# Optimization experiments

Hardware: AMD Instinct MI355X
Metric: run time of the kernel (lower is better)

The kernel has to match this reference:

```python
import jax, jax.numpy as jnp
import numpy as np

B, D_IN, T = 16, 1024, 4096
CB_SIZE, CB_DIM = 8192, 512
EPS = 1e-12


def _conv1d_s2(x, w):
    # x: [b, c_in, t], w: [c_out, c_in, 3]; stride 2, padding 1 (matches nn.Conv1d)
    return jax.lax.conv_general_dilated(
        x, w, window_strides=(2,), padding=[(1, 1)],
        dimension_numbers=("NCH", "OIH", "NCH"))


def _l2_normalize(v):
    # F.normalize(v, dim=1) semantics
    return v / jnp.maximum(jnp.linalg.norm(v, axis=1, keepdims=True), EPS)


def setup_inputs() -> dict:
    key = jax.random.key(0)
    k1, k2, k3, k4 = jax.random.split(key, 4)
    x = jax.random.normal(k1, (B, D_IN, T), dtype=jnp.float32)
    w1 = jax.random.normal(k2, (CB_DIM, D_IN, 3), dtype=jnp.float32) * 0.02
    w2 = jax.random.normal(k3, (CB_DIM, CB_DIM, 3), dtype=jnp.float32) * 0.02
    codebook = jax.random.normal(k4, (CB_SIZE, CB_DIM), dtype=jnp.float32)
    return {"x": x, "w1": w1, "w2": w2, "codebook": codebook}


def reference(x, w1, w2, codebook):
    # in_proj: two stride-2 convs -> [b, cb_dim, t], t = T // 4
    x_e = _conv1d_s2(_conv1d_s2(x, w1), w2)
    b, d, t = x_e.shape
    enc = x_e.transpose(0, 2, 1).reshape(b * t, d)   # (b t) d
    enc = _l2_normalize(enc)
    cb = _l2_normalize(codebook)
    # squared euclidean distance via matmul
    dist = (jnp.sum(enc * enc, axis=1, keepdims=True)
            - 2.0 * enc @ cb.T
            + jnp.sum(cb * cb, axis=1)[None, :])     # (b t) codebook_size
    indices = jnp.argmax(-dist, axis=1).reshape(b, t)
    return indices
```

## Files before the change

### kernel.cpp

```cpp
#include <hip/hip_runtime.h>


typedef __attribute__((ext_vector_type(8))) _Float16 f16x8;
typedef __attribute__((ext_vector_type(8))) short bf16x8;
typedef __attribute__((ext_vector_type(4))) float f32x4;

__device__ inline ushort f2bf(float x) {
  union { float f; unsigned u; } v; v.f = x;
  unsigned r = v.u + 0x7fffu + ((v.u >> 16) & 1u);
  return (ushort)(r >> 16);
}

__device__ inline void splitf(float v, ushort& h, ushort& l) {
  union { _Float16 h; ushort u; } a, b;
  a.h = (_Float16)v;
  b.h = (_Float16)(v - (float)a.h);
  h = a.u; l = b.u;
}

__global__ __launch_bounds__(256) void prep_w(const float* __restrict__ w,
                                              ushort* __restrict__ ws,
                                              int n ) {
  const int idx = blockIdx.x * 256 + threadIdx.x;
  if (idx >= n) return;
  const float v0 = w[(size_t)idx * 3 + 0];
  const float v1 = w[(size_t)idx * 3 + 1];
  const float v2 = w[(size_t)idx * 3 + 2];
  ushort h, l;
  splitf(v0, h, l); ws[idx] = h; ws[(size_t)n + idx] = l;
  splitf(v1, h, l); ws[2 * (size_t)n + idx] = h; ws[3 * (size_t)n + idx] = l;
  splitf(v2, h, l); ws[4 * (size_t)n + idx] = h; ws[5 * (size_t)n + idx] = l;
}

template <int C_IN, int T_IN, int T_OUT, bool TOUT>
__global__ __launch_bounds__(256, 3) void conv_mfma(
    const float* __restrict__ x, const ushort* __restrict__ ws,
    float* __restrict__ out) {
  const int co0 = blockIdx.x * 128;
  const int t0 = blockIdx.y * 128;
  const int b = blockIdx.z;
  const int tid = threadIdx.x;
  const int wv = tid >> 6;
  const int lane = tid & 63;
  const int l15 = lane & 15, quad = lane >> 4;

  constexpr int PX = 40;
  __shared__ ushort xe_hi[128 * PX], xe_lo[128 * PX];
  __shared__ ushort xo_hi[130 * PX], xo_lo[130 * PX];

  f32x4 acc[2][8] = {};
  const float* xb = x + (size_t)b * C_IN * T_IN;

  for (int ci0 = 0; ci0 < C_IN; ci0 += 32) {
    __syncthreads();
    {
      const int cg = tid & 3, tf = tid >> 2;
#pragma unroll
      for (int r = 0; r < 8; r++) {
        const int ci = cg * 8 + r;
        const float* xp = xb + (size_t)(ci0 + ci) * T_IN + 2 * t0 + 4 * tf;
        const float4 v = *(const float4*)xp;
        ushort h, l;
        splitf(v.x, h, l); xe_hi[(2 * tf) * PX + ci] = h; xe_lo[(2 * tf) * PX + ci] = l;
        splitf(v.y, h, l); xo_hi[(2 * tf + 1) * PX + ci] = h; xo_lo[(2 * tf + 1) * PX + ci] = l;
        splitf(v.z, h, l); xe_hi[(2 * tf + 1) * PX + ci] = h; xe_lo[(2 * tf + 1) * PX + ci] = l;
        splitf(v.w, h, l); xo_hi[(2 * tf + 2) * PX + ci] = h; xo_lo[(2 * tf + 2) * PX + ci] = l;
        if (tf == 0) {
          const float v0 = (t0 > 0) ? xp[-1] : 0.0f;
          splitf(v0, h, l); xo_hi[ci] = h; xo_lo[ci] = l;
        }
      }
    }
    __syncthreads();

#pragma unroll
    for (int koff = 0; koff < 3; koff++) {
      f16x8 a_h[2], a_l[2];
#pragma unroll
      for (int i = 0; i < 2; i++) {
        const size_t co = (size_t)co0 + wv * 32 + i * 16 + l15;
        const ushort* wp = ws + ((size_t)(koff * 2) * 512 + co) * C_IN + ci0 + quad * 8;
        a_h[i] = *(const f16x8*)wp;
        a_l[i] = *(const f16x8*)(wp + (size_t)512 * C_IN);
      }
      const ushort* bh_arr = (koff == 1) ? xe_hi : xo_hi;
      const ushort* bl_arr = (koff == 1) ? xe_lo : xo_lo;
      const int radd = (koff == 2) ? 1 : 0;
#pragma unroll
      for (int j = 0; j < 8; j++) {
        const int row = j * 16 + l15 + radd;
        const f16x8 b_h = *(const f16x8*)(bh_arr + row * PX + quad * 8);
        const f16x8 b_l = *(const f16x8*)(bl_arr + row * PX + quad * 8);
#pragma unroll
        for (int i = 0; i < 2; i++) {
          acc[i][j] = __builtin_amdgcn_mfma_f32_16x16x32_f16(a_h[i], b_h, acc[i][j], 0, 0, 0);
          acc[i][j] = __builtin_amdgcn_mfma_f32_16x16x32_f16(a_h[i], b_l, acc[i][j], 0, 0, 0);
          acc[i][j] = __builtin_amdgcn_mfma_f32_16x16x32_f16(a_l[i], b_h, acc[i][j], 0, 0, 0);
        }
      }
    }
  }

#pragma unroll
  for (int i = 0; i < 2; i++) {
#pragma unroll
    for (int j = 0; j < 8; j++) {
      const int t = t0 + j * 16 + l15;
      const int co = co0 + wv * 32 + i * 16 + quad * 4;
      if (TOUT) {
        const float4 v = make_float4(acc[i][j][0], acc[i][j][1], acc[i][j][2], acc[i][j][3]);
        *(float4*)(out + ((size_t)b * T_OUT + t) * 512 + co) = v;
      } else {
#pragma unroll
        for (int r = 0; r < 4; r++)
          out[((size_t)b * 512 + co + r) * T_OUT + t] = acc[i][j][r];
      }
    }
  }
}

__global__ __launch_bounds__(64) void norm_rows(const float* __restrict__ out2t,
                                                float* __restrict__ enc,
                                                ushort* __restrict__ enc16) {
  const int row = blockIdx.x;
  const int lane = threadIdx.x;
  const float* p = out2t + (size_t)row * 512 + lane * 8;
  const float4 v0 = *(const float4*)p;
  const float4 v1 = *(const float4*)(p + 4);
  float ss = v0.x * v0.x + v0.y * v0.y + v0.z * v0.z + v0.w * v0.w +
             v1.x * v1.x + v1.y * v1.y + v1.z * v1.z + v1.w * v1.w;
#pragma unroll
  for (int m = 32; m >= 1; m >>= 1) ss += __shfl_xor(ss, m, 64);
  const float inv = 1.0f / fmaxf(sqrtf(ss), 1e-12f);
  float4 a, c;
  a.x = v0.x * inv; a.y = v0.y * inv; a.z = v0.z * inv; a.w = v0.w * inv;
  c.x = v1.x * inv; c.y = v1.y * inv; c.z = v1.z * inv; c.w = v1.w * inv;
  float* eo = enc + (size_t)row * 512 + lane * 8;
  *(float4*)eo = a;
  *(float4*)(eo + 4) = c;
  ushort u[8] = {f2bf(a.x), f2bf(a.y), f2bf(a.z), f2bf(a.w),
                 f2bf(c.x), f2bf(c.y), f2bf(c.z), f2bf(c.w)};
  *(uint4*)(enc16 + (size_t)row * 512 + lane * 8) = *(const uint4*)u;
}

__global__ __launch_bounds__(256) void norm_cb(const float* __restrict__ cb,
                                               float* __restrict__ cbn,
                                               ushort* __restrict__ cbn16,
                                               float* __restrict__ cb2) {
  const int row = blockIdx.x * 4 + (threadIdx.x >> 6);
  const int lane = threadIdx.x & 63;
  const float* p = cb + (long)row * 512;
  const float4 v0 = *(const float4*)(p + lane * 4);
  const float4 v1 = *(const float4*)(p + 256 + lane * 4);
  float ss = v0.x * v0.x + v0.y * v0.y + v0.z * v0.z + v0.w * v0.w +
             v1.x * v1.x + v1.y * v1.y + v1.z * v1.z + v1.w * v1.w;
#pragma unroll
  for (int m = 32; m >= 1; m >>= 1) ss += __shfl_xor(ss, m, 64);
  const float n = fmaxf(sqrtf(ss), 1e-12f);
  float4 a, c;
  a.x = v0.x / n; a.y = v0.y / n; a.z = v0.z / n; a.w = v0.w / n;
  c.x = v1.x / n; c.y = v1.y / n; c.z = v1.z / n; c.w = v1.w / n;
  *(float4*)(cbn + (long)row * 512 + lane * 4) = a;
  *(float4*)(cbn + (long)row * 512 + 256 + lane * 4) = c;
  ushort4 ua, uc;
  ua.x = f2bf(a.x); ua.y = f2bf(a.y); ua.z = f2bf(a.z); ua.w = f2bf(a.w);
  uc.x = f2bf(c.x); uc.y = f2bf(c.y); uc.z = f2bf(c.z); uc.w = f2bf(c.w);
  *(ushort4*)(cbn16 + (long)row * 512 + lane * 4) = ua;
  *(ushort4*)(cbn16 + (long)row * 512 + 256 + lane * 4) = uc;
  float s2 = a.x * a.x + a.y * a.y + a.z * a.z + a.w * a.w +
             c.x * c.x + c.y * c.y + c.z * c.z + c.w * c.w;
#pragma unroll
  for (int m = 32; m >= 1; m >>= 1) s2 += __shfl_xor(s2, m, 64);
  if (lane == 0) cb2[row] = s2;
}

__device__ inline void top2_merge(float& s1, int& i1, float& s2, int& i2,
                                  float t1, int j1, float t2, int j2) {
  if (t1 > s1) {
    if (s1 > t2) { s2 = s1; i2 = i1; } else { s2 = t2; i2 = j2; }
    s1 = t1; i1 = j1;
  } else if (t1 > s2) {
    s2 = t1; i2 = j1;
  }
}

__global__ __launch_bounds__(256) void score_top2(
    const ushort* __restrict__ enc16, const ushort* __restrict__ cbn16,
    const float* __restrict__ cb2, float* __restrict__ pscore,
    int* __restrict__ pidx) {
  const int nt = blockIdx.x;
  const int mt = blockIdx.y;
  const int m0 = mt * 128, n0 = nt * 128;
  const int tid = threadIdx.x;
  const int wave = tid >> 6, lane = tid & 63;
  const int wm = wave & 1, wn = wave >> 1;
  const int quad = lane >> 4, l15 = lane & 15;

  __shared__ ushort a_s[128 * 72];
  __shared__ ushort b_s[128 * 72];

  f32x4 acc[4][4] = {};

  for (int k0 = 0; k0 < 512; k0 += 64) {
#pragma unroll
    for (int q = 0; q < 4; q++) {
      const int chunk = tid + 256 * q;
      const int row = chunk >> 3, kb = chunk & 7;
      const uint4 va = *(const uint4*)(enc16 + (size_t)(m0 + row) * 512 + k0 + kb * 8);
      *(uint4*)(a_s + row * 72 + kb * 8) = va;
      const uint4 vb = *(const uint4*)(cbn16 + (size_t)(n0 + row) * 512 + k0 + kb * 8);
      *(uint4*)(b_s + row * 72 + kb * 8) = vb;
    }
    __syncthreads();
#pragma unroll
    for (int kk = 0; kk < 2; kk++) {
      bf16x8 af[4], bf[4];
#pragma unroll
      for (int i = 0; i < 4; i++)
        af[i] = *(const bf16x8*)(a_s + (wm * 64 + i * 16 + l15) * 72 + kk * 32 + quad * 8);
#pragma unroll
      for (int j = 0; j < 4; j++)
        bf[j] = *(const bf16x8*)(b_s + (wn * 64 + j * 16 + l15) * 72 + kk * 32 + quad * 8);
#pragma unroll
      for (int i = 0; i < 4; i++)
#pragma unroll
        for (int j = 0; j < 4; j++)
          acc[i][j] = __builtin_amdgcn_mfma_f32_16x16x32_bf16(af[i], bf[j], acc[i][j], 0, 0, 0);
    }
    __syncthreads();
  }

  float cb2c[4];
  int coln[4];
#pragma unroll
  for (int j = 0; j < 4; j++) {
    coln[j] = n0 + wn * 64 + j * 16 + l15;
    cb2c[j] = cb2[coln[j]];
  }

#pragma unroll
  for (int mi = 0; mi < 4; mi++) {
#pragma unroll
    for (int i = 0; i < 4; i++) {
      float s1 = -3.4e38f, s2 = -3.4e38f;
      int i1 = -1, i2 = -1;
#pragma unroll
      for (int j = 0; j < 4; j++) {
        const float s = 2.0f * acc[mi][j][i] - cb2c[j];
        if (s > s1) { s2 = s1; i2 = i1; s1 = s; i1 = coln[j]; }
        else if (s > s2) { s2 = s; i2 = coln[j]; }
      }
#pragma unroll
      for (int m = 8; m >= 1; m >>= 1) {
        const float t1 = __shfl_xor(s1, m, 64);
        const int j1 = __shfl_xor(i1, m, 64);
        const float t2 = __shfl_xor(s2, m, 64);
        const int j2 = __shfl_xor(i2, m, 64);
        top2_merge(s1, i1, s2, i2, t1, j1, t2, j2);
      }
      if (l15 == 0) {
        const int row_g = m0 + wm * 64 + mi * 16 + quad * 4 + i;
        const size_t base = (size_t)row_g * 256 + (size_t)nt * 4 + wn * 2;
        pscore[base] = s1; pidx[base] = i1;
        pscore[base + 1] = s2; pidx[base + 1] = i2;
      }
    }
  }
}

__global__ __launch_bounds__(256) void rescore_argmax(
    const float* __restrict__ enc, const float* __restrict__ cbn,
    const float* __restrict__ cb2, const float* __restrict__ pscore,
    const int* __restrict__ pidx, int* __restrict__ out) {
  const int row = blockIdx.x;
  const int tid = threadIdx.x;
  __shared__ float wbest[4];
  __shared__ int wslot[4];
  __shared__ int winner;
  __shared__ int cand[8];
  __shared__ float fsc[8];
  __shared__ int fid[8];

  float s = pscore[(size_t)row * 256 + tid];
  const int id = pidx[(size_t)row * 256 + tid];

  for (int it = 0; it < 8; it++) {
    float bs = s;
    int bslot = tid;
#pragma unroll
    for (int m = 32; m >= 1; m >>= 1) {
      const float os = __shfl_xor(bs, m, 64);
      const int oslot = __shfl_xor(bslot, m, 64);
      if (os > bs || (os == bs && oslot < bslot)) { bs = os; bslot = oslot; }
    }
    if ((tid & 63) == 0) { wbest[tid >> 6] = bs; wslot[tid >> 6] = bslot; }
    __syncthreads();
    if (tid == 0) {
      float b = wbest[0]; int sl = wslot[0];
      for (int wv = 1; wv < 4; wv++)
        if (wbest[wv] > b || (wbest[wv] == b && wslot[wv] < sl)) { b = wbest[wv]; sl = wslot[wv]; }
      winner = sl;
    }
    __syncthreads();
    if (tid == winner) { cand[it] = id; s = -3.4e38f; }
    __syncthreads();
  }

  const int c = cand[tid >> 5];
  const float* ep = enc + (size_t)row * 512;
  const float* cp = cbn + (size_t)c * 512;
  float dot = 0.0f;
  const int d0 = (tid & 31) * 16;
#pragma unroll
  for (int u = 0; u < 4; u++) {
    const float4 e4 = *(const float4*)(ep + d0 + u * 4);
    const float4 c4 = *(const float4*)(cp + d0 + u * 4);
    dot = fmaf(e4.x, c4.x, dot);
    dot = fmaf(e4.y, c4.y, dot);
    dot = fmaf(e4.z, c4.z, dot);
    dot = fmaf(e4.w, c4.w, dot);
  }
#pragma unroll
  for (int m = 16; m >= 1; m >>= 1) dot += __shfl_xor(dot, m, 64);
  if ((tid & 31) == 0) {
    fsc[tid >> 5] = 2.0f * dot - cb2[c];
    fid[tid >> 5] = c;
  }
  __syncthreads();
  if (tid == 0) {
    float b = fsc[0]; int bi = fid[0];
    for (int q = 1; q < 8; q++)
      if (fsc[q] > b || (fsc[q] == b && fid[q] < bi)) { b = fsc[q]; bi = fid[q]; }
    out[row] = bi;
  }
}

extern "C" void kernel_launch(void* const* d_in, const int* in_sizes, int n_in,
                              void* d_out, int out_size, void* d_ws, size_t ws_size,
                              hipStream_t stream) {
  const float* x = (const float*)d_in[0];
  const float* w1 = (const float*)d_in[1];
  const float* w2 = (const float*)d_in[2];
  const float* cb = (const float*)d_in[3];
  int* out = (int*)d_out;

  char* w0 = (char*)d_ws;
  float* out1 = (float*)w0;
  ushort* enc16 = (ushort*)w0;
  float* pscore = (float*)(w0 + (16ull << 20));
  int* pidx = (int*)(w0 + (32ull << 20));
  float* out2t = (float*)(w0 + (64ull << 20));
  float* enc = (float*)(w0 + (96ull << 20));
  float* cbn = (float*)(w0 + (128ull << 20));
  ushort* cbn16 = (ushort*)(w0 + (144ull << 20));
  float* cb2 = (float*)(w0 + (152ull << 20));
  ushort* ws1 = (ushort*)(w0 + (153ull << 20));
  ushort* ws2 = (ushort*)(w0 + (159ull << 20));

  prep_w<<<2048, 256, 0, stream>>>(w1, ws1, 512 * 1024);
  prep_w<<<1024, 256, 0, stream>>>(w2, ws2, 512 * 512);
  conv_mfma<1024, 4096, 2048, false><<<dim3(4, 16, 16), 256, 0, stream>>>(x, ws1, out1);
  conv_mfma<512, 2048, 1024, true><<<dim3(4, 8, 16), 256, 0, stream>>>(out1, ws2, out2t);
  norm_rows<<<16384, 64, 0, stream>>>(out2t, enc, enc16);
  norm_cb<<<2048, 256, 0, stream>>>(cb, cbn, cbn16, cb2);
  score_top2<<<dim3(64, 128), 256, 0, stream>>>(enc16, cbn16, cb2, pscore, pidx);
  rescore_argmax<<<16384, 256, 0, stream>>>(enc, cbn, cb2, pscore, pidx, out);
}
```

Baseline: 1.917 ms.

## Pre-split conv inputs into fp16 hi/lo even/odd layout and shrink time tile

```diff
diff --git a/kernel.cpp b/kernel.cpp
--- a/kernel.cpp
+++ b/kernel.cpp
@@ -32,43 +32,92 @@
   splitf(v2, h, l); ws[4 * (size_t)n + idx] = h; ws[5 * (size_t)n + idx] = l;
 }
 
-template <int C_IN, int T_IN, int T_OUT, bool TOUT>
-__global__ __launch_bounds__(256, 3) void conv_mfma(
-    const float* __restrict__ x, const ushort* __restrict__ ws,
-    float* __restrict__ out) {
-  const int co0 = blockIdx.x * 128;
-  const int t0 = blockIdx.y * 128;
+__global__ __launch_bounds__(256) void zero_halo(ushort* __restrict__ xo1,
+                                                 ushort* __restrict__ xo2) {
+  const int b = blockIdx.x, tid = threadIdx.x;
+  const uint4 z = make_uint4(0, 0, 0, 0);
+  *(uint4*)(xo1 + (size_t)b * 2049 * 2048 + tid * 8) = z;
+  if (tid < 128) *(uint4*)(xo2 + (size_t)b * 1025 * 1024 + tid * 8) = z;
+}
+
+template <int CI, int T>
+__global__ __launch_bounds__(256) void prep_x(const float* __restrict__ x,
+                                              ushort* __restrict__ xe,
+                                              ushort* __restrict__ xo) {
+  const int t0 = blockIdx.x * 256;
+  const int ci0 = blockIdx.y * 32;
   const int b = blockIdx.z;
   const int tid = threadIdx.x;
-  const int wv = tid >> 6;
-  const int lane = tid & 63;
+  __shared__ float tile[32][257];
+  const int wv = tid >> 6, lane = tid & 63;
+  const float* xb = x + ((size_t)b * CI + ci0) * T + t0;
+#pragma unroll
+  for (int r = 0; r < 8; r++) {
+    const int ci = r * 4 + wv;
+    const float4 v = *(const float4*)(xb + (size_t)ci * T + lane * 4);
+    tile[ci][lane * 4 + 0] = v.x; tile[ci][lane * 4 + 1] = v.y;
+    tile[ci][lane * 4 + 2] = v.z; tile[ci][lane * 4 + 3] = v.w;
+  }
+  __syncthreads();
+  const int jj = tid >> 1, ph = tid & 1;
+  const int tl = 2 * jj + ph;
+  __attribute__((aligned(16))) ushort h[32], l[32];
+#pragma unroll
+  for (int c = 0; c < 32; c++) splitf(tile[c][tl], h[c], l[c]);
+  constexpr int TH = T / 2;
+  constexpr int RW = CI * 2;
+  ushort* dst;
+  if (ph == 0) dst = xe + ((size_t)b * TH + (t0 >> 1) + jj) * RW;
+  else dst = xo + ((size_t)b * (TH + 1) + (t0 >> 1) + jj + 1) * RW;
+  dst += (ci0 >> 5) * 64;
+#pragma unroll
+  for (int k = 0; k < 4; k++) {
+    *(uint4*)(dst + k * 8) = *(const uint4*)(h + k * 8);
+    *(uint4*)(dst + 32 + k * 8) = *(const uint4*)(l + k * 8);
+  }
+}
+
+template <int C_IN, int T_OUT, bool SPLIT_OUT>
+__global__ __launch_bounds__(256, 4) void conv_mfma(
+    const ushort* __restrict__ xe, const ushort* __restrict__ xo,
+    const ushort* __restrict__ ws, float* __restrict__ out,
+    ushort* __restrict__ ye, ushort* __restrict__ yo) {
+  const int co0 = blockIdx.x * 128;
+  const int t0 = blockIdx.y * 64;
+  const int b = blockIdx.z;
+  const int tid = threadIdx.x;
+  const int wv = tid >> 6, lane = tid & 63;
   const int l15 = lane & 15, quad = lane >> 4;
 
-  constexpr int PX = 40;
-  __shared__ ushort xe_hi[128 * PX], xe_lo[128 * PX];
-  __shared__ ushort xo_hi[130 * PX], xo_lo[130 * PX];
-
-  f32x4 acc[2][8] = {};
-  const float* xb = x + (size_t)b * C_IN * T_IN;
+  __shared__ ushort xeh[64 * 40], xel[64 * 40], xoh[65 * 40], xol[65 * 40];
+
+  f32x4 acc[2][4] = {};
+  const int RW = C_IN * 2;
+  const ushort* xe_b = xe + ((size_t)b * T_OUT + t0) * RW;
+  const ushort* xo_b = xo + ((size_t)b * (T_OUT + 1) + t0) * RW;
 
   for (int ci0 = 0; ci0 < C_IN; ci0 += 32) {
     __syncthreads();
-    {
-      const int cg = tid & 3, tf = tid >> 2;
-#pragma unroll
-      for (int r = 0; r < 8; r++) {
-        const int ci = cg * 8 + r;
-        const float* xp = xb + (size_t)(ci0 + ci) * T_IN + 2 * t0 + 4 * tf;
-        const float4 v = *(const float4*)xp;
-        ushort h, l;
-        splitf(v.x, h, l); xe_hi[(2 * tf) * PX + ci] = h; xe_lo[(2 * tf) * PX + ci] = l;
-        splitf(v.y, h, l); xo_hi[(2 * tf + 1) * PX + ci] = h; xo_lo[(2 * tf + 1) * PX + ci] = l;
-        splitf(v.z, h, l); xe_hi[(2 * tf + 1) * PX + ci] = h; xe_lo[(2 * tf + 1) * PX + ci] = l;
-        splitf(v.w, h, l); xo_hi[(2 * tf + 2) * PX + ci] = h; xo_lo[(2 * tf + 2) * PX + ci] = l;
-        if (tf == 0) {
-          const float v0 = (t0 > 0) ? xp[-1] : 0.0f;
-          splitf(v0, h, l); xo_hi[ci] = h; xo_lo[ci] = l;
+    const int choff = (ci0 >> 5) * 64;
+#pragma unroll
+    for (int q = 0; q < 5; q++) {
+      const int id = tid + 256 * q;
+      if (id < 1032) {
+        const int g = id & 3;
+        const int u = id >> 2;
+        const uint4* src;
+        ushort* dst;
+        if (u < 128) {
+          const int row = u >> 1, part = u & 1;
+          src = (const uint4*)(xe_b + (size_t)row * RW + choff + part * 32 + g * 8);
+          dst = (part ? xel : xeh) + row * 40 + g * 8;
+        } else {
+          const int u2 = u - 128;
+          const int row = u2 >> 1, part = u2 & 1;
+          src = (const uint4*)(xo_b + (size_t)row * RW + choff + part * 32 + g * 8);
+          dst = (part ? xol : xoh) + row * 40 + g * 8;
         }
+        *(uint4*)dst = *src;
       }
     }
     __syncthreads();
@@ -79,18 +128,18 @@
 #pragma unroll
       for (int i = 0; i < 2; i++) {
         const size_t co = (size_t)co0 + wv * 32 + i * 16 + l15;
-        const ushort* wp = ws + ((size_t)(koff * 2) * 512 + co) * C_IN + ci0 + quad * 8;
+        const ushort* wp = ws + ((size_t)(koff * 2) * 512) * C_IN + co * C_IN + ci0 + quad * 8;
         a_h[i] = *(const f16x8*)wp;
         a_l[i] = *(const f16x8*)(wp + (size_t)512 * C_IN);
       }
-      const ushort* bh_arr = (koff == 1) ? xe_hi : xo_hi;
-      const ushort* bl_arr = (koff == 1) ? xe_lo : xo_lo;
+      const ushort* bh = (koff == 1) ? xeh : xoh;
+      const ushort* bl = (koff == 1) ? xel : xol;
       const int radd = (koff == 2) ? 1 : 0;
 #pragma unroll
-      for (int j = 0; j < 8; j++) {
+      for (int j = 0; j < 4; j++) {
         const int row = j * 16 + l15 + radd;
-        const f16x8 b_h = *(const f16x8*)(bh_arr + row * PX + quad * 8);
-        const f16x8 b_l = *(const f16x8*)(bl_arr + row * PX + quad * 8);
+        const f16x8 b_h = *(const f16x8*)(bh + row * 40 + quad * 8);
+        const f16x8 b_l = *(const f16x8*)(bl + row * 40 + quad * 8);
 #pragma unroll
         for (int i = 0; i < 2; i++) {
           acc[i][j] = __builtin_amdgcn_mfma_f32_16x16x32_f16(a_h[i], b_h, acc[i][j], 0, 0, 0);
@@ -101,19 +150,34 @@
     }
   }
 
-#pragma unroll
-  for (int i = 0; i < 2; i++) {
-#pragma unroll
-    for (int j = 0; j < 8; j++) {
-      const int t = t0 + j * 16 + l15;
-      const int co = co0 + wv * 32 + i * 16 + quad * 4;
-      if (TOUT) {
+  if (SPLIT_OUT) {
+#pragma unroll
+    for (int i = 0; i < 2; i++) {
+      const int ch = (co0 >> 5) + wv;
+      const int ci32 = i * 16 + quad * 4;
+#pragma unroll
+      for (int j = 0; j < 4; j++) {
+        const int t = t0 + j * 16 + l15;
+        const int ph = t & 1;
+        const int row = (t >> 1) + ph;
+        __attribute__((aligned(8))) ushort h[4], l[4];
+#pragma unroll
+        for (int r = 0; r < 4; r++) splitf(acc[i][j][r], h[r], l[r]);
+        ushort* dst = (ph ? yo : ye) +
+                      ((size_t)b * (ph ? 1025 : 1024) + row) * 1024 + ch * 64 + ci32;
+        *(uint2*)dst = *(const uint2*)h;
+        *(uint2*)(dst + 32) = *(const uint2*)l;
+      }
+    }
+  } else {
+#pragma unroll
+    for (int i = 0; i < 2; i++) {
+#pragma unroll
+      for (int j = 0; j < 4; j++) {
+        const int t = t0 + j * 16 + l15;
+        const int co = co0 + wv * 32 + i * 16 + quad * 4;
         const float4 v = make_float4(acc[i][j][0], acc[i][j][1], acc[i][j][2], acc[i][j][3]);
         *(float4*)(out + ((size_t)b * T_OUT + t) * 512 + co) = v;
-      } else {
-#pragma unroll
-        for (int r = 0; r < 4; r++)
-          out[((size_t)b * 512 + co + r) * T_OUT + t] = acc[i][j][r];
       }
     }
   }
@@ -138,8 +202,9 @@
   float* eo = enc + (size_t)row * 512 + lane * 8;
   *(float4*)eo = a;
   *(float4*)(eo + 4) = c;
-  ushort u[8] = {f2bf(a.x), f2bf(a.y), f2bf(a.z), f2bf(a.w),
-                 f2bf(c.x), f2bf(c.y), f2bf(c.z), f2bf(c.w)};
+  __attribute__((aligned(16))) ushort u[8] = {
+      f2bf(a.x), f2bf(a.y), f2bf(a.z), f2bf(a.w),
+      f2bf(c.x), f2bf(c.y), f2bf(c.z), f2bf(c.w)};
   *(uint4*)(enc16 + (size_t)row * 512 + lane * 8) = *(const uint4*)u;
 }
 
@@ -345,22 +410,30 @@
   int* out = (int*)d_out;
 
   char* w0 = (char*)d_ws;
-  float* out1 = (float*)w0;
-  ushort* enc16 = (ushort*)w0;
-  float* pscore = (float*)(w0 + (16ull << 20));
-  int* pidx = (int*)(w0 + (32ull << 20));
-  float* out2t = (float*)(w0 + (64ull << 20));
-  float* enc = (float*)(w0 + (96ull << 20));
-  float* cbn = (float*)(w0 + (128ull << 20));
-  ushort* cbn16 = (ushort*)(w0 + (144ull << 20));
-  float* cb2 = (float*)(w0 + (152ull << 20));
-  ushort* ws1 = (ushort*)(w0 + (153ull << 20));
-  ushort* ws2 = (ushort*)(w0 + (159ull << 20));
-
+  const size_t MB = 1ull << 20;
+  ushort* xe1 = (ushort*)(w0);
+  ushort* xo1 = (ushort*)(w0 + 128 * MB);
+  ushort* xe2 = (ushort*)(w0 + 257 * MB);
+  ushort* xo2 = (ushort*)(w0 + 289 * MB);
+  ushort* ws1 = (ushort*)(w0 + 322 * MB);
+  ushort* ws2 = (ushort*)(w0 + 328 * MB);
+  float* out2t = (float*)(w0);
+  float* enc = (float*)(w0 + 32 * MB);
+  ushort* enc16 = (ushort*)(w0 + 64 * MB);
+  float* cbn = (float*)(w0 + 80 * MB);
+  ushort* cbn16 = (ushort*)(w0 + 96 * MB);
+  float* cb2 = (float*)(w0 + 104 * MB);
+  float* pscore = (float*)(w0 + 112 * MB);
+  int* pidx = (int*)(w0 + 128 * MB);
+
+  zero_halo<<<16, 256, 0, stream>>>(xo1, xo2);
   prep_w<<<2048, 256, 0, stream>>>(w1, ws1, 512 * 1024);
   prep_w<<<1024, 256, 0, stream>>>(w2, ws2, 512 * 512);
-  conv_mfma<1024, 4096, 2048, false><<<dim3(4, 16, 16), 256, 0, stream>>>(x, ws1, out1);
-  conv_mfma<512, 2048, 1024, true><<<dim3(4, 8, 16), 256, 0, stream>>>(out1, ws2, out2t);
+  prep_x<1024, 4096><<<dim3(16, 32, 16), 256, 0, stream>>>(x, xe1, xo1);
+  conv_mfma<1024, 2048, true><<<dim3(4, 32, 16), 256, 0, stream>>>(
+      xe1, xo1, ws1, nullptr, xe2, xo2);
+  conv_mfma<512, 1024, false><<<dim3(4, 16, 16), 256, 0, stream>>>(
+      xe2, xo2, ws2, out2t, nullptr, nullptr);
   norm_rows<<<16384, 64, 0, stream>>>(out2t, enc, enc16);
   norm_cb<<<2048, 256, 0, stream>>>(cb, cbn, cbn16, cb2);
   score_top2<<<dim3(64, 128), 256, 0, stream>>>(enc16, cbn16, cb2, pscore, pidx);
```

Result: faster. 1.748 ms (-8.8%).
